# Kernel optimization log

Measured on AMD Instinct MI355X. Metric: run time of the kernel, lower is better.

The kernel has to match this reference:

```python
import jax, jax.numpy as jnp
import numpy as np

VOCAB, EMBED, TOPICS, NDOCS = 30000, 200, 100, 2048
DT_ALPHA, TW_ALPHA = 3.0, 2.0
EPS_OT = 1e-16   # ETP sinkhorn epsilon
EPS_LOG = 1e-12  # FASTopic self.epsilon
N_SINKHORN_ITERS = 100  # fixed iteration count (original: while err>thr and cpt<max_iter)


def pairwise_sqeuclidean(x, y):
    return (jnp.sum(x * x, axis=1, keepdims=True)
            + jnp.sum(y * y, axis=1)
            - 2.0 * (x @ y.T))


def sinkhorn_etp(x, y, a, b, alpha):
    # Entropic OT between point clouds x:[n,d], y:[m,d]; a:[n,1], b:[m,1] marginals.
    M = pairwise_sqeuclidean(x, y)          # [n, m]
    K = jnp.exp(-alpha * M)                  # Gibbs kernel
    u0 = jnp.full_like(a, 1.0 / a.shape[0])

    def step(carry, _):
        u, _v = carry
        v = b / (K.T @ u + EPS_OT)           # [m,1]
        u = a / (K @ v + EPS_OT)             # [n,1]
        return (u, v), None

    (u, v), _ = jax.lax.scan(step, (u0, jnp.zeros_like(b)), None, length=N_SINKHORN_ITERS)
    transp = u * (K * v.T)                   # [n, m] transport plan
    loss = jnp.sum(transp * M)
    return loss, transp


def setup_inputs() -> dict:
    key = jax.random.key(0)
    k1, k2, k3, k4 = jax.random.split(key, 4)
    # word_embeddings: trunc_normal(std=1) then L2-row-normalize
    we = jax.random.truncated_normal(k1, -2.0, 2.0, (VOCAB, EMBED), jnp.float32)
    we = we / jnp.linalg.norm(we, axis=1, keepdims=True)
    # topic_embeddings: trunc_normal(std=0.1) then L2-row-normalize
    te = 0.1 * jax.random.truncated_normal(k2, -2.0, 2.0, (TOPICS, EMBED), jnp.float32)
    te = te / jnp.linalg.norm(te, axis=1, keepdims=True)
    word_weights = jnp.full((VOCAB, 1), 1.0 / VOCAB, jnp.float32)
    topic_weights = jnp.full((TOPICS, 1), 1.0 / TOPICS, jnp.float32)
    train_bow = jax.random.uniform(k3, (NDOCS, VOCAB), jnp.float32)
    doc_embeddings = jax.random.normal(k4, (NDOCS, EMBED), jnp.float32)
    return {
        "train_bow": train_bow,
        "doc_embeddings": doc_embeddings,
        "word_embeddings": we,
        "topic_embeddings": te,
        "word_weights": word_weights,
        "topic_weights": topic_weights,
    }


def reference(train_bow, doc_embeddings, word_embeddings, topic_embeddings,
              word_weights, topic_weights):
    n_docs = doc_embeddings.shape[0]
    n_topics = topic_embeddings.shape[0]
    # DT_ETP: a uniform over docs, b = softmax(topic_weights)
    a_dt = jnp.full((n_docs, 1), 1.0 / n_docs, doc_embeddings.dtype)
    b_dt = jax.nn.softmax(topic_weights, axis=0)
    loss_DT, transp_DT = sinkhorn_etp(doc_embeddings, topic_embeddings, a_dt, b_dt, DT_ALPHA)
    # TW_ETP: a uniform over topics, b = softmax(word_weights)
    a_tw = jnp.full((n_topics, 1), 1.0 / n_topics, topic_embeddings.dtype)
    b_tw = jax.nn.softmax(word_weights, axis=0)
    loss_TW, transp_TW = sinkhorn_etp(topic_embeddings, word_embeddings, a_tw, b_tw, TW_ALPHA)

    loss_ETP = loss_DT + loss_TW
    theta = transp_DT * n_docs               # [N, K]
    beta = transp_TW * n_topics              # [K, V]
    recon = theta @ beta                     # [N, V]
    loss_DSR = -jnp.mean(jnp.sum(train_bow * jnp.log(recon + EPS_LOG), axis=1))
    loss = loss_DSR + loss_ETP
    return loss, loss_DSR, loss_ETP
```

## Files before the change

kernel.cpp:

```cpp
#include <hip/hip_runtime.h>
#include <math.h>

#define V 30000
#define E 200
#define T 100
#define N 2048
#define NITER 100
#define KSTR 112
#define EPS_OT 1e-16f
#define EPS_LOG 1e-12f

#define NBTW 40
#define WPT 3
#define NDT 8
#define PSTR 64

#define OFF_KTW    0
#define OFF_KDT    1680000
#define OFF_WW     1884800
#define OFF_DD     1914800
#define OFF_TT     1916848
#define OFF_PM     1916976
#define OFF_PS     1917104
#define OFF_BTW    1917232
#define OFF_BDT    1947232
#define OFF_ACC    1947360
#define OFF_ACCDT  1957360
#define OFF_VTW    1967360
#define OFF_UDT    1997360
#define OFF_UTW    1999408
#define OFF_VDT    1999536
#define OFF_DBL    1999664
#define OFF_FLAG   1999680
#define OFF_KDTNZ  1999681
#define OFF_ARR    1999682
#define OFF_PART   2000000

#define LOBF(u) __uint_as_float((u) << 16)
#define HIBF(u) __uint_as_float((u) & 0xffff0000u)

typedef __attribute__((ext_vector_type(4))) float f32x4;

__device__ __forceinline__ unsigned short f2bf(float f) {
    unsigned int u = __float_as_uint(f);
    return (unsigned short)((u + 0x7fffu + ((u >> 16) & 1u)) >> 16);
}
__device__ __forceinline__ float bf2f(unsigned short h) {
    return __uint_as_float(((unsigned int)h) << 16);
}

__device__ __forceinline__ float brsum(float x, float* red8) {
    int tid = threadIdx.x;
    for (int o = 32; o; o >>= 1) x += __shfl_down(x, o, 64);
    __syncthreads();
    if ((tid & 63) == 0) red8[tid >> 6] = x;
    __syncthreads();
    return (red8[0] + red8[1]) + (red8[2] + red8[3]);
}

__device__ __forceinline__ void load_krow(const unsigned short* kg, int j, unsigned* ku) {
    const uint4* kp = (const uint4*)(kg + (size_t)j * KSTR);
    #pragma unroll
    for (int i = 0; i < 12; i++) {
        uint4 q = kp[i];
        ku[4*i] = q.x; ku[4*i+1] = q.y; ku[4*i+2] = q.z; ku[4*i+3] = q.w;
    }
    uint2 q2 = *(const uint2*)(((const unsigned*)kp) + 48);
    ku[48] = q2.x; ku[49] = q2.y;
}

__device__ __forceinline__ f32x4 ldg_coh4(const float* p) {
    f32x4 r;
    asm volatile("global_load_dwordx4 %0, %1, off sc0 sc1" : "=v"(r) : "v"(p) : "memory");
    return r;
}
__device__ __forceinline__ void stg_coh1(float* p, float v) {
    asm volatile("global_store_dword %0, %1, off sc0 sc1" :: "v"(p), "v"(v) : "memory");
}
__device__ __forceinline__ void wait_vm0() {
    asm volatile("s_waitcnt vmcnt(0)" ::: "memory");
    __builtin_amdgcn_sched_barrier(0);
}

__device__ __forceinline__ float poll_sum20(const float* Pp, unsigned ptag) {
    f32x4 a0, a1, a2, a3, a4;
    while (true) {
        a0 = ldg_coh4(Pp + 0);
        a1 = ldg_coh4(Pp + 4);
        a2 = ldg_coh4(Pp + 8);
        a3 = ldg_coh4(Pp + 12);
        a4 = ldg_coh4(Pp + 16);
        wait_vm0();
        unsigned u0x = __float_as_uint(a0.x), u0y = __float_as_uint(a0.y),
                 u0z = __float_as_uint(a0.z), u0w = __float_as_uint(a0.w);
        unsigned u1x = __float_as_uint(a1.x), u1y = __float_as_uint(a1.y),
                 u1z = __float_as_uint(a1.z), u1w = __float_as_uint(a1.w);
        unsigned u2x = __float_as_uint(a2.x), u2y = __float_as_uint(a2.y),
                 u2z = __float_as_uint(a2.z), u2w = __float_as_uint(a2.w);
        unsigned u3x = __float_as_uint(a3.x), u3y = __float_as_uint(a3.y),
                 u3z = __float_as_uint(a3.z), u3w = __float_as_uint(a3.w);
        unsigned u4x = __float_as_uint(a4.x), u4y = __float_as_uint(a4.y),
                 u4z = __float_as_uint(a4.z), u4w = __float_as_uint(a4.w);
        unsigned and_ = u0x & u0y & u0z & u0w & u1x & u1y & u1z & u1w
                      & u2x & u2y & u2z & u2w & u3x & u3y & u3z & u3w
                      & u4x & u4y & u4z & u4w;
        unsigned or_  = u0x | u0y | u0z | u0w | u1x | u1y | u1z | u1w
                      | u2x | u2y | u2z | u2w | u3x | u3y | u3z | u3w
                      | u4x | u4y | u4z | u4w;
        if (ptag ? (and_ >> 31) : !(or_ >> 31)) break;
        __builtin_amdgcn_s_sleep(1);
    }
    return (((fabsf(a0.x) + fabsf(a0.y)) + (fabsf(a0.z) + fabsf(a0.w)))
          + ((fabsf(a1.x) + fabsf(a1.y)) + (fabsf(a1.z) + fabsf(a1.w))))
         + (((fabsf(a2.x) + fabsf(a2.y)) + (fabsf(a2.z) + fabsf(a2.w)))
          + ((fabsf(a3.x) + fabsf(a3.y)) + (fabsf(a3.z) + fabsf(a3.w))))
         + ((fabsf(a4.x) + fabsf(a4.y)) + (fabsf(a4.z) + fabsf(a4.w)));
}

__device__ __forceinline__ void gbar(int* ctr, int n, int tid) {
    __syncthreads();
    if (tid == 0) {
        __hip_atomic_fetch_add(ctr, 1, __ATOMIC_RELEASE, __HIP_MEMORY_SCOPE_AGENT);
        while (__hip_atomic_load(ctr, __ATOMIC_ACQUIRE, __HIP_MEMORY_SCOPE_AGENT) < n)
            __builtin_amdgcn_s_sleep(1);
    }
    __syncthreads();
}

__device__ __forceinline__ float agent_ldf(const float* p) {
    return __hip_atomic_load(p, __ATOMIC_RELAXED, __HIP_MEMORY_SCOPE_AGENT);
}

__global__ void k_pre(const float* __restrict__ we, const float* __restrict__ de,
                      const float* __restrict__ te, const float* __restrict__ wwgt,
                      const float* __restrict__ twgt, float* ws) {
    __shared__ float red[256];
    int tid = threadIdx.x, b = blockIdx.x;
    int gid = b * 256 + tid;
    if (gid < 2 * NITER * T) ws[OFF_ACC + gid] = 0.f;
    if (gid < 16) ws[OFF_DBL + gid] = 0.f;
    if (gid < 2) ((int*)ws)[OFF_FLAG + gid] = 0;
    if (gid < 2 * NITER) ((int*)ws)[OFF_ARR + gid] = 0;
    if (gid < 2 * T * PSTR) ws[OFF_PART + gid] = __uint_as_float(0x80000000u);
    {
        int r = gid;
        const float* src = nullptr; float* dst = nullptr; int row = 0;
        if (r < V)              { src = we; dst = ws + OFF_WW; row = r; }
        else if (r < V + N)     { src = de; dst = ws + OFF_DD; row = r - V; }
        else if (r < V + N + T) { src = te; dst = ws + OFF_TT; row = r - V - N; }
        if (src) {
            const float4* p = (const float4*)(src + (size_t)row * E);
            float s = 0.f;
            #pragma unroll 10
            for (int i = 0; i < E / 4; i++) { float4 v = p[i]; s += v.x*v.x + v.y*v.y + v.z*v.z + v.w*v.w; }
            dst[row] = s;
        }
    }
    if (b < 118) {
        int j = gid;
        float w = (j < V) ? wwgt[j] : -INFINITY;
        red[tid] = w; __syncthreads();
        for (int s = 128; s > 0; s >>= 1) { if (tid < s) red[tid] = fmaxf(red[tid], red[tid + s]); __syncthreads(); }
        float m = red[0]; __syncthreads();
        float e = (j < V) ? expf(w - m) : 0.f;
        red[tid] = e; __syncthreads();
        for (int s = 128; s > 0; s >>= 1) { if (tid < s) red[tid] += red[tid + s]; __syncthreads(); }
        if (tid == 0) { ws[OFF_PM + b] = m; ws[OFF_PS + b] = red[0]; }
    } else if (b == 120) {
        float w = (tid < T) ? twgt[tid] : -INFINITY;
        red[tid] = w; __syncthreads();
        for (int s = 128; s > 0; s >>= 1) { if (tid < s) red[tid] = fmaxf(red[tid], red[tid + s]); __syncthreads(); }
        float m = red[0]; __syncthreads();
        float e = (tid < T) ? expf(w - m) : 0.f;
        red[tid] = e; __syncthreads();
        for (int s = 128; s > 0; s >>= 1) { if (tid < s) red[tid] += red[tid + s]; __syncthreads(); }
        if (tid < T) ws[OFF_BDT + tid] = e / red[0];
    }
}

__global__ void k_pre2(const float* __restrict__ wwgt, float* ws) {
    __shared__ float red[128];
    int tid = threadIdx.x, b = blockIdx.x;
    float m = (tid < 118) ? ws[OFF_PM + tid] : -INFINITY;
    if (tid < 128) red[tid] = m;
    __syncthreads();
    for (int s = 64; s > 0; s >>= 1) { if (tid < s) red[tid] = fmaxf(red[tid], red[tid + s]); __syncthreads(); }
    float mw = red[0]; __syncthreads();
    float p = (tid < 118) ? ws[OFF_PS + tid] * expf(ws[OFF_PM + tid] - mw) : 0.f;
    if (tid < 128) red[tid] = p;
    __syncthreads();
    for (int s = 64; s > 0; s >>= 1) { if (tid < s) red[tid] += red[tid + s]; __syncthreads(); }
    float Sw = red[0];
    int j = b * 256 + tid;
    if (j < V) ws[OFF_BTW + j] = expf(wwgt[j] - mw) / Sw;
}

__global__ void k_ktw(const float* __restrict__ we, const float* __restrict__ te, float* ws) {
    __shared__ float wt[8][256];
    __shared__ float tp[8][25];
    __shared__ float tts[25];
    int tid = threadIdx.x;
    int j0 = blockIdx.x * 256;
    int t0 = blockIdx.y * 25;
    int j = j0 + tid;
    int jl = (j < V) ? j : V - 1;
    float acc[25];
    #pragma unroll
    for (int i = 0; i < 25; i++) acc[i] = 0.f;
    if (tid < 25) tts[tid] = ws[OFF_TT + t0 + tid];
    for (int kk = 0; kk < E; kk += 8) {
        #pragma unroll
        for (int k = 0; k < 8; k++) wt[k][tid] = we[(size_t)jl * E + kk + k];
        if (tid < 200) { int i = tid >> 3; int k = tid & 7; tp[k][i] = te[(size_t)(t0 + i) * E + kk + k]; }
        __syncthreads();
        #pragma unroll
        for (int k = 0; k < 8; k++) {
            float w = wt[k][tid];
            #pragma unroll
            for (int i = 0; i < 25; i++) acc[i] += tp[k][i] * w;
        }
        __syncthreads();
    }
    if (j < V) {
        float wwj = ws[OFF_WW + j];
        unsigned short* kg = (unsigned short*)(ws + OFF_KTW);
        #pragma unroll
        for (int i = 0; i < 25; i++) {
            float M = tts[i] + wwj - 2.f * acc[i];
            kg[(size_t)j * KSTR + t0 + i] = f2bf(expf(-2.f * M));
        }
    }
}

__global__ void k_kdt(const float* __restrict__ de, const float* __restrict__ te, float* ws) {
    int gid = blockIdx.x * 256 + threadIdx.x;
    if (gid >= N * T) return;
    int n = gid / T; int t = gid - n * T;
    const float4* dp  = (const float4*)(de + (size_t)n * E);
    const float4* tpp = (const float4*)(te + (size_t)t * E);
    float s = 0.f;
    #pragma unroll 10
    for (int i = 0; i < E / 4; i++) { float4 a = dp[i], b = tpp[i]; s += a.x*b.x + a.y*b.y + a.z*b.z + a.w*b.w; }
    float M = ws[OFF_DD + n] + ws[OFF_TT + t] - 2.f * s;
    float kv = expf(-3.f * M);
    ws[OFF_KDT + gid] = kv;
    unsigned long long m = __ballot(kv != 0.f);
    if (m && (threadIdx.x & 63) == 0) atomicOr(((int*)ws) + OFF_KDTNZ, 1);
}

__global__ __launch_bounds__(256, 1) void k_sink(const float* __restrict__ bow, float* ws) {
    __shared__ float sm[256 * 26];
    __shared__ float pr[256];
    __shared__ float u_sh[100];
    __shared__ float red8[8];
    int tid = threadIdx.x, b = blockIdx.x;

    if (b >= NBTW && b < NBTW + 128) {
        const float4* b4 = (const float4*)bow;
        for (int k = 0; k < 96; k++) {
            size_t base = (size_t)k * 160000;
            float s = 0.f;
            for (int i = (b - NBTW) * 256 + tid; i < 160000; i += 128 * 256) {
                float4 x = b4[base + i]; s += (x.x + x.y) + (x.z + x.w);
            }
            float bs = brsum(s, red8);
            if (tid == 0) atomicAdd((double*)(ws + OFF_DBL) + 3, (double)bs);
        }
        return;
    }

    if (b >= NBTW + 128) {
        if (((volatile int*)ws)[OFF_KDTNZ] == 0) return;
        int* arr = ((int*)ws) + OFF_ARR;
        int d = (b - (NBTW + 128)) * 256 + tid;
        const float* Kr = ws + OFF_KDT + (size_t)d * T;
        for (int k = 0; k < NITER; k++) {
            if (tid < T) u_sh[tid] = (k == 0) ? 0.f
                : ws[OFF_BDT + tid] / (agent_ldf(ws + OFF_ACCDT + (k - 1) * T + tid) + EPS_OT);
            __syncthreads();
            float u;
            if (k == 0) u = 1.f / N;
            else {
                float s = 0.f;
                #pragma unroll 4
                for (int t = 0; t < T; t++) s += Kr[t] * u_sh[t];
                u = (1.f / N) / (s + EPS_OT);
            }
            #pragma unroll
            for (int c = 0; c < 4; c++) {
                #pragma unroll
                for (int i = 0; i < 25; i++) sm[tid * 26 + i] = Kr[25 * c + i] * u;
                __syncthreads();
                int g = tid >> 5, tl = tid & 31;
                float s2 = 0.f;
                if (tl < 25) {
                    #pragma unroll 8
                    for (int q = 0; q < 32; q++) s2 += sm[(g * 32 + q) * 26 + tl];
                }
                pr[g * 32 + tl] = s2;
                __syncthreads();
                if (tid < 25) {
                    float r = 0.f;
                    #pragma unroll
                    for (int g2 = 0; g2 < 8; g2++) r += pr[g2 * 32 + tid];
                    atomicAdd(&ws[OFF_ACCDT + k * T + 25 * c + tid], r);
                }
                __syncthreads();
            }
            gbar(arr + NITER + k, NDT, tid);
        }
        if (tid < T) {
            float vf = ws[OFF_BDT + tid] / (agent_ldf(ws + OFF_ACCDT + (NITER - 1) * T + tid) + EPS_OT);
            u_sh[tid] = vf;
            if (b == NBTW + 128) ws[OFF_VDT + tid] = vf;
        }
        __syncthreads();
        float s = 0.f;
        #pragma unroll 4
        for (int t = 0; t < T; t++) s += Kr[t] * u_sh[t];
        float u = (1.f / N) / (s + EPS_OT);
        ws[OFF_UDT + d] = u;
        float ld = 0.f; int nz = 0;
        for (int t = 0; t < T; t++) {
            float kv = Kr[t];
            if (kv > 0.f) ld += u * kv * u_sh[t] * (-(1.f / 3.f) * logf(kv));
            if ((float)N * u * kv * u_sh[t] != 0.f) nz = 1;
        }
        float ldb = brsum(ld, red8);
        if (tid == 0) atomicAdd((double*)(ws + OFF_DBL) + 1, (double)ldb);
        if (nz) atomicOr(((int*)ws) + OFF_FLAG, 1);
        return;
    }

    const unsigned short* kg = (const unsigned short*)(ws + OFF_KTW);
    unsigned ku[WPT][50];
    float bj[WPT];
    #pragma unroll
    for (int w = 0; w < WPT; w++) {
        int j = (b * WPT + w) * 256 + tid;
        bool oob = (j >= V);
        load_krow(kg, oob ? V - 1 : j, ku[w]);
        if (oob) {
            #pragma unroll
            for (int q = 0; q < 50; q++) ku[w][q] = 0;
        }
        bj[w] = oob ? 0.f : ws[OFF_BTW + j];
    }
    float v[WPT];
    #pragma unroll
    for (int w = 0; w < WPT; w++) v[w] = 0.f;

    for (int k = 0; k < NITER; k++) {
        if (k == 0) {
            if (tid < T) u_sh[tid] = 0.01f;
        } else {
            float rs = 0.f;
            if (tid < 2 * T) {
                int t = tid >> 1, half = tid & 1;
                const float* Pp = ws + OFF_PART + (size_t)((k - 1) & 1) * (T * PSTR)
                                  + t * PSTR + half * 20;
                rs = poll_sum20(Pp, ((k - 1) >> 1) & 1);
            }
            pr[tid] = rs;
            __syncthreads();
            if (tid < T) u_sh[tid] = 0.01f / ((pr[2 * tid] + pr[2 * tid + 1]) + EPS_OT);
        }
        __syncthreads();
        #pragma unroll
        for (int w = 0; w < WPT; w++) {
            float s = 0.f;
            #pragma unroll
            for (int q = 0; q < 50; q++)
                s += LOBF(ku[w][q]) * u_sh[2 * q] + HIBF(ku[w][q]) * u_sh[2 * q + 1];
            v[w] = bj[w] / (s + EPS_OT);
        }
        if (k == NITER - 1) {
            #pragma unroll
            for (int w = 0; w < WPT; w++) {
                int j = (b * WPT + w) * 256 + tid;
                if (j < V) ws[OFF_VTW + j] = v[w];
            }
        }
        float* Pw = ws + OFF_PART + (size_t)(k & 1) * (T * PSTR);
        unsigned wsign = (unsigned)((k >> 1) & 1) << 31;
        #pragma unroll
        for (int c = 0; c < 4; c++) {
            #pragma unroll
            for (int i = 0; i < 25; i++) {
                int t = 25 * c + i;
                float p = 0.f;
                #pragma unroll
                for (int w = 0; w < WPT; w++) {
                    unsigned wu = ku[w][t >> 1];
                    float kt = (t & 1) ? HIBF(wu) : LOBF(wu);
                    p += kt * v[w];
                }
                sm[tid * 26 + i] = p;
            }
            __syncthreads();
            int g = tid >> 5, tl = tid & 31;
            float s2 = 0.f;
            if (tl < 25) {
                #pragma unroll 8
                for (int q = 0; q < 32; q++) s2 += sm[(g * 32 + q) * 26 + tl];
            }
            pr[g * 32 + tl] = s2;
            __syncthreads();
            if (tid < 25) {
                float r = 0.f;
                #pragma unroll
                for (int g2 = 0; g2 < 8; g2++) r += pr[g2 * 32 + tid];
                stg_coh1(Pw + (25 * c + tid) * PSTR + b,
                         __uint_as_float(__float_as_uint(r) | wsign));
            }
            __syncthreads();
        }
    }
    {
        float rs = 0.f;
        if (tid < 2 * T) {
            int t = tid >> 1, half = tid & 1;
            const float* Pp = ws + OFF_PART + (size_t)((NITER - 1) & 1) * (T * PSTR)
                              + t * PSTR + half * 20;
            rs = poll_sum20(Pp, ((NITER - 1) >> 1) & 1);
        }
        pr[tid] = rs;
        __syncthreads();
        if (tid < T) {
            float uf = 0.01f / ((pr[2 * tid] + pr[2 * tid + 1]) + EPS_OT);
            u_sh[tid] = uf;
            if (b == 0) ws[OFF_UTW + tid] = uf;
        }
    }
    __syncthreads();
    float lt = 0.f;
    #pragma unroll
    for (int w = 0; w < WPT; w++) {
        int j = (b * WPT + w) * 256 + tid;
        if (j < V) {
            #pragma unroll
            for (int q = 0; q < 50; q++) {
                float k0 = LOBF(ku[w][q]), k1 = HIBF(ku[w][q]);
                if (k0 > 0.f) lt += u_sh[2 * q]     * k0 * v[w] * (-0.5f * logf(k0));
                if (k1 > 0.f) lt += u_sh[2 * q + 1] * k1 * v[w] * (-0.5f * logf(k1));
            }
        }
    }
    float ltb = brsum(lt, red8);
    if (tid == 0) atomicAdd((double*)(ws + OFF_DBL) + 2, (double)ltb);
}

__global__ void k_dsr(const float* __restrict__ bow, float* ws) {
    if (*(volatile int*)(((int*)ws) + OFF_FLAG) == 0) return;
    __shared__ float th[32 * T];
    __shared__ float u2[T];
    __shared__ float vd[T];
    __shared__ float red[256];
    __shared__ int flag;
    int tid = threadIdx.x;
    int j0 = blockIdx.x * 256;
    int d0 = blockIdx.y * 32;
    if (tid < T) { vd[tid] = ws[OFF_VDT + tid]; u2[tid] = ws[OFF_UTW + tid]; }
    if (tid == 0) flag = 0;
    __syncthreads();
    bool nz = false;
    for (int idx = tid; idx < 32 * T; idx += 256) {
        int dl = idx / T; int t = idx - dl * T;
        float thv = (float)N * ws[OFF_UDT + d0 + dl] * ws[OFF_KDT + (size_t)(d0 + dl) * T + t] * vd[t];
        th[idx] = thv;
        nz |= (thv != 0.f);
    }
    if (nz) flag = 1;
    __syncthreads();
    int j = j0 + tid;
    float part = 0.f;
    const unsigned short* kg = (const unsigned short*)(ws + OFF_KTW);
    if (flag) {
        float acc[32];
        #pragma unroll
        for (int d = 0; d < 32; d++) acc[d] = 0.f;
        if (j < V) {
            float vj = ws[OFF_VTW + j];
            for (int t = 0; t < T; t++) {
                float kv = bf2f(kg[(size_t)j * KSTR + t]);
                float beta = (float)T * u2[t] * kv * vj;
                #pragma unroll
                for (int d = 0; d < 32; d++) acc[d] += th[d * T + t] * beta;
            }
            for (int d = 0; d < 32; d++)
                part += bow[(size_t)(d0 + d) * V + j] * logf(acc[d] + EPS_LOG);
        }
    } else {
        if (j < V) {
            float sb = 0.f;
            #pragma unroll 8
            for (int d = 0; d < 32; d++) sb += bow[(size_t)(d0 + d) * V + j];
            part = sb * logf(EPS_LOG);
        }
    }
    red[tid] = part; __syncthreads();
    for (int s = 128; s > 0; s >>= 1) { if (tid < s) red[tid] += red[tid + s]; __syncthreads(); }
    if (tid == 0) atomicAdd((double*)(ws + OFF_DBL) + 0, (double)red[0]);
}

__global__ void k_finish(float* ws, float* out) {
    if (threadIdx.x == 0 && blockIdx.x == 0) {
        double* dbl = (double*)(ws + OFF_DBL);
        int flag = ((int*)ws)[OFF_FLAG];
        double dsr_sum = flag ? dbl[0] : dbl[3] * (double)logf(EPS_LOG);
        double ldsr = -dsr_sum / (double)N;
        double letp = dbl[1] + dbl[2];
        out[0] = (float)(ldsr + letp);
        out[1] = (float)ldsr;
        out[2] = (float)letp;
    }
}

extern "C" void kernel_launch(void* const* d_in, const int* in_sizes, int n_in,
                              void* d_out, int out_size, void* d_ws, size_t ws_size,
                              hipStream_t stream) {
    const float* bow  = (const float*)d_in[0];
    const float* de   = (const float*)d_in[1];
    const float* we   = (const float*)d_in[2];
    const float* te   = (const float*)d_in[3];
    const float* wwgt = (const float*)d_in[4];
    const float* twgt = (const float*)d_in[5];
    float* out = (float*)d_out;
    float* ws  = (float*)d_ws;

    k_pre<<<128, 256, 0, stream>>>(we, de, te, wwgt, twgt, ws);
    k_pre2<<<118, 256, 0, stream>>>(wwgt, ws);
    k_ktw<<<dim3(118, 4), 256, 0, stream>>>(we, te, ws);
    k_kdt<<<800, 256, 0, stream>>>(de, te, ws);
    k_sink<<<NBTW + 128 + NDT, 256, 0, stream>>>(bow, ws);
    k_dsr<<<dim3(118, 64), 256, 0, stream>>>(bow, ws);
    k_finish<<<1, 64, 0, stream>>>(ws, out);
}
```

Before: 1.318 ms.

## Add dedicated aggregator block that reduces topic partials and broadcasts u vector

```diff
diff --git a/kernel.cpp b/kernel.cpp
--- a/kernel.cpp
+++ b/kernel.cpp
@@ -35,6 +35,7 @@
 #define OFF_KDTNZ  1999681
 #define OFF_ARR    1999682
 #define OFF_PART   2000000
+#define OFF_UARR   2013000
 
 #define LOBF(u) __uint_as_float((u) << 16)
 #define HIBF(u) __uint_as_float((u) & 0xffff0000u)
@@ -76,6 +77,9 @@
 }
 __device__ __forceinline__ void stg_coh1(float* p, float v) {
     asm volatile("global_store_dword %0, %1, off sc0 sc1" :: "v"(p), "v"(v) : "memory");
+}
+__device__ __forceinline__ void stg_coh4(float* p, f32x4 v) {
+    asm volatile("global_store_dwordx4 %0, %1, off sc0 sc1" :: "v"(p), "v"(v) : "memory");
 }
 __device__ __forceinline__ void wait_vm0() {
     asm volatile("s_waitcnt vmcnt(0)" ::: "memory");
@@ -117,6 +121,21 @@
          + ((fabsf(a4.x) + fabsf(a4.y)) + (fabsf(a4.z) + fabsf(a4.w)));
 }
 
+__device__ __forceinline__ f32x4 poll_u4(const float* p, unsigned ptag) {
+    f32x4 a;
+    while (true) {
+        a = ldg_coh4(p);
+        wait_vm0();
+        unsigned ax = __float_as_uint(a.x), ay = __float_as_uint(a.y),
+                 az = __float_as_uint(a.z), aw = __float_as_uint(a.w);
+        unsigned and_ = ax & ay & az & aw;
+        unsigned or_  = ax | ay | az | aw;
+        if (ptag ? (and_ >> 31) : !(or_ >> 31)) break;
+        __builtin_amdgcn_s_sleep(1);
+    }
+    return a;
+}
+
 __device__ __forceinline__ void gbar(int* ctr, int n, int tid) {
     __syncthreads();
     if (tid == 0) {
@@ -142,6 +161,7 @@
     if (gid < 2) ((int*)ws)[OFF_FLAG + gid] = 0;
     if (gid < 2 * NITER) ((int*)ws)[OFF_ARR + gid] = 0;
     if (gid < 2 * T * PSTR) ws[OFF_PART + gid] = __uint_as_float(0x80000000u);
+    if (gid < 256) ws[OFF_UARR + gid] = (gid < 128) ? 0.f : __uint_as_float(0x80000000u);
     {
         int r = gid;
         const float* src = nullptr; float* dst = nullptr; int row = 0;
@@ -269,7 +289,7 @@
         return;
     }
 
-    if (b >= NBTW + 128) {
+    if (b >= NBTW + 128 && b < NBTW + 128 + NDT) {
         if (((volatile int*)ws)[OFF_KDTNZ] == 0) return;
         int* arr = ((int*)ws) + OFF_ARR;
         int d = (b - (NBTW + 128)) * 256 + tid;
@@ -332,6 +352,33 @@
         return;
     }
 
+    if (b >= NBTW + 128 + NDT) {
+        for (int k = 1; k <= NITER; k++) {
+            float rs = 0.f;
+            if (tid < 2 * T) {
+                int t = tid >> 1, half = tid & 1;
+                const float* Pp = ws + OFF_PART + (size_t)((k - 1) & 1) * (T * PSTR)
+                                  + t * PSTR + half * 20;
+                rs = poll_sum20(Pp, ((k - 1) >> 1) & 1);
+            }
+            pr[tid] = rs;
+            __syncthreads();
+            if (tid < T) u_sh[tid] = 0.01f / ((pr[2 * tid] + pr[2 * tid + 1]) + EPS_OT);
+            __syncthreads();
+            unsigned usign = (unsigned)((k >> 1) & 1) << 31;
+            if (tid < 25) {
+                f32x4 uv;
+                uv.x = __uint_as_float(__float_as_uint(u_sh[4 * tid + 0]) | usign);
+                uv.y = __uint_as_float(__float_as_uint(u_sh[4 * tid + 1]) | usign);
+                uv.z = __uint_as_float(__float_as_uint(u_sh[4 * tid + 2]) | usign);
+                uv.w = __uint_as_float(__float_as_uint(u_sh[4 * tid + 3]) | usign);
+                stg_coh4(ws + OFF_UARR + (size_t)(k & 1) * 128 + 4 * tid, uv);
+            }
+            __syncthreads();
+        }
+        return;
+    }
+
     const unsigned short* kg = (const unsigned short*)(ws + OFF_KTW);
     unsigned ku[WPT][50];
     float bj[WPT];
@@ -353,17 +400,12 @@
     for (int k = 0; k < NITER; k++) {
         if (k == 0) {
             if (tid < T) u_sh[tid] = 0.01f;
-        } else {
-            float rs = 0.f;
-            if (tid < 2 * T) {
-                int t = tid >> 1, half = tid & 1;
-                const float* Pp = ws + OFF_PART + (size_t)((k - 1) & 1) * (T * PSTR)
-                                  + t * PSTR + half * 20;
-                rs = poll_sum20(Pp, ((k - 1) >> 1) & 1);
-            }
-            pr[tid] = rs;
-            __syncthreads();
-            if (tid < T) u_sh[tid] = 0.01f / ((pr[2 * tid] + pr[2 * tid + 1]) + EPS_OT);
+        } else if (tid < 25) {
+            f32x4 a = poll_u4(ws + OFF_UARR + (size_t)(k & 1) * 128 + 4 * tid, (k >> 1) & 1);
+            u_sh[4 * tid + 0] = fabsf(a.x);
+            u_sh[4 * tid + 1] = fabsf(a.y);
+            u_sh[4 * tid + 2] = fabsf(a.z);
+            u_sh[4 * tid + 3] = fabsf(a.w);
         }
         __syncthreads();
         #pragma unroll
@@ -416,23 +458,15 @@
             __syncthreads();
         }
     }
-    {
-        float rs = 0.f;
-        if (tid < 2 * T) {
-            int t = tid >> 1, half = tid & 1;
-            const float* Pp = ws + OFF_PART + (size_t)((NITER - 1) & 1) * (T * PSTR)
-                              + t * PSTR + half * 20;
-            rs = poll_sum20(Pp, ((NITER - 1) >> 1) & 1);
-        }
-        pr[tid] = rs;
-        __syncthreads();
-        if (tid < T) {
-            float uf = 0.01f / ((pr[2 * tid] + pr[2 * tid + 1]) + EPS_OT);
-            u_sh[tid] = uf;
-            if (b == 0) ws[OFF_UTW + tid] = uf;
-        }
-    }
-    __syncthreads();
+    if (tid < 25) {
+        f32x4 a = poll_u4(ws + OFF_UARR + (size_t)(NITER & 1) * 128 + 4 * tid, (NITER >> 1) & 1);
+        u_sh[4 * tid + 0] = fabsf(a.x);
+        u_sh[4 * tid + 1] = fabsf(a.y);
+        u_sh[4 * tid + 2] = fabsf(a.z);
+        u_sh[4 * tid + 3] = fabsf(a.w);
+    }
+    __syncthreads();
+    if (b == 0 && tid < T) ws[OFF_UTW + tid] = u_sh[tid];
     float lt = 0.f;
     #pragma unroll
     for (int w = 0; w < WPT; w++) {
@@ -532,7 +566,7 @@
     k_pre2<<<118, 256, 0, stream>>>(wwgt, ws);
     k_ktw<<<dim3(118, 4), 256, 0, stream>>>(we, te, ws);
     k_kdt<<<800, 256, 0, stream>>>(de, te, ws);
-    k_sink<<<NBTW + 128 + NDT, 256, 0, stream>>>(bow, ws);
+    k_sink<<<NBTW + 128 + NDT + 1, 256, 0, stream>>>(bow, ws);
     k_dsr<<<dim3(118, 64), 256, 0, stream>>>(bow, ws);
     k_finish<<<1, 64, 0, stream>>>(ws, out);
 }
```

After: 1.213 ms (median of 2 runs). 8.0% less time.
